# Kernel optimization log

Measured on AMD Instinct MI355X. Metric: run time of the kernel, lower is better.

## Reference

```python
import jax, jax.numpy as jnp
import numpy as np

B, V, K = 4, 4096, 128
C_IN, C_W, C_OUT, N_BLOCK = 16, 128, 128, 4
MLP_C = 3 * C_W  # x_in | x_diffuse | grad_features


def setup_inputs() -> dict:
    key = jax.random.key(0)
    ks = jax.random.split(key, 24)
    inp = {
        'x_in': jax.random.normal(ks[0], (B, V, C_IN), jnp.float32),
        'mass': jax.random.uniform(ks[1], (B, V), jnp.float32, 0.1, 1.0),
        'evals': jax.random.uniform(ks[2], (B, K), jnp.float32, 0.0, 50.0),
        'evecs': jax.random.normal(ks[3], (B, V, K), jnp.float32) / np.sqrt(V),
        'gradX': jax.random.normal(ks[4], (B, V, V), jnp.float32) * 0.01,
        'gradY': jax.random.normal(ks[5], (B, V, V), jnp.float32) * 0.01,
        # network parameters
        'Wf': jax.random.normal(ks[6], (C_IN, C_W), jnp.float32) / np.sqrt(C_IN),
        'bf': jnp.zeros((C_W,), jnp.float32),
        'Wl': jax.random.normal(ks[7], (C_W, C_OUT), jnp.float32) / np.sqrt(C_W),
        'bl': jnp.zeros((C_OUT,), jnp.float32),
        't': jax.random.uniform(ks[8], (N_BLOCK, C_W), jnp.float32, 0.0, 1.0),
        'Are': jax.random.normal(ks[9], (N_BLOCK, C_W, C_W), jnp.float32) / np.sqrt(C_W),
        'Aim': jax.random.normal(ks[10], (N_BLOCK, C_W, C_W), jnp.float32) / np.sqrt(C_W),
        'W0': jax.random.normal(ks[11], (N_BLOCK, MLP_C, C_W), jnp.float32) / np.sqrt(MLP_C),
        'b0': jnp.zeros((N_BLOCK, C_W), jnp.float32),
        'W1': jax.random.normal(ks[12], (N_BLOCK, C_W, C_W), jnp.float32) / np.sqrt(C_W),
        'b1': jnp.zeros((N_BLOCK, C_W), jnp.float32),
        'W2': jax.random.normal(ks[13], (N_BLOCK, C_W, C_W), jnp.float32) / np.sqrt(C_W),
        'b2': jnp.zeros((N_BLOCK, C_W), jnp.float32),
    }
    return inp


def _forward(x_in, mass, evals, evecs, gradX, gradY,
             Wf, bf, Wl, bl, t, Are, Aim, W0, b0, W1, b1, W2, b2):
    x = x_in @ Wf + bf  # [B,V,C]
    for i in range(N_BLOCK):
        # --- learned-time spectral diffusion ---
        ti = jnp.maximum(t[i], 1e-8)                                  # [C]
        x_spec = jnp.einsum('bvk,bvc->bkc', evecs, x * mass[..., None])  # to_basis
        coefs = jnp.exp(-evals[..., None] * ti)                       # [B,K,C]
        x_diff = jnp.einsum('bvk,bkc->bvc', evecs, coefs * x_spec)    # from_basis
        # --- spatial gradient features (per-batch grad operator matmuls) ---
        gx = jnp.einsum('bvw,bwc->bvc', gradX, x_diff)
        gy = jnp.einsum('bvw,bwc->bvc', gradY, x_diff)
        # complex-linear: (A_re + i A_im)(gx + i gy); torch Linear y = x W^T,
        # here weights are stored pre-transposed so y = x @ W.
        br = gx @ Are[i] - gy @ Aim[i]
        bi = gy @ Are[i] + gx @ Aim[i]
        gfeat = jnp.tanh(gx * br + gy * bi)                           # [B,V,C]
        # --- vertex MLP with residual (dropout inactive at inference) ---
        f = jnp.concatenate([x, x_diff, gfeat], axis=-1)              # [B,V,3C]
        h = jax.nn.relu(f @ W0[i] + b0[i])
        h = jax.nn.relu(h @ W1[i] + b1[i])
        h = h @ W2[i] + b2[i]
        x = x + h
    return x @ Wl + bl  # [B,V,C_OUT], outputs_at='vertices', no last_activation


def reference(x_in, mass, evals, evecs, gradX, gradY,
              Wf, bf, Wl, bl, t, Are, Aim, W0, b0, W1, b1, W2, b2):
    return _forward(x_in, mass, evals, evecs, gradX, gradY,
                    Wf, bf, Wl, bl, t, Are, Aim, W0, b0, W1, b1, W2, b2)
```

## Files before the change

### kernel.cpp

```cpp
#include <hip/hip_runtime.h>
#include <stdint.h>
#include <math.h>


typedef unsigned short u16;
typedef __attribute__((ext_vector_type(8))) short short8;
typedef __attribute__((ext_vector_type(8))) __bf16 bf16x8;
typedef __attribute__((ext_vector_type(4))) float f32x4;

#define B_ 4
#define V_ 4096
#define K_ 128
#define C_ 128

__device__ __forceinline__ float bf2f(u16 u) {
    union { unsigned i; float f; } v; v.i = ((unsigned)u) << 16; return v.f;
}
__device__ __forceinline__ u16 f2bf(float f) {
    union { float f; unsigned i; } v; v.f = f;
    unsigned u = v.i;
    return (u16)((u + 0x7fffu + ((u >> 16) & 1u)) >> 16);
}

__device__ __forceinline__ f32x4 mfma16(short8 a, short8 b, f32x4 c) {
    return __builtin_amdgcn_mfma_f32_16x16x32_bf16(
        __builtin_bit_cast(bf16x8, a), __builtin_bit_cast(bf16x8, b), c, 0, 0, 0);
}

__device__ __forceinline__ void gl_lds16(const u16* g, u16* l) {
    __builtin_amdgcn_global_load_lds(
        (const __attribute__((address_space(1))) unsigned*)g,
        (__attribute__((address_space(3))) unsigned*)l, 16, 0, 0);
}

template <int RT>
__device__ __forceinline__ void gemm_core(const u16* A, int lda,
                                          const u16* Bt, int ldbt, int kIters,
                                          f32x4 (&acc)[RT][4], u16* As, u16* Bs) {
    const int tid = threadIdx.x;
    const int lane = tid & 63, wave = tid >> 6;
    const int rb = (wave >> 1) * (RT * 16), cb = (wave & 1) * 64;
    const int lrow = lane >> 3;
    const int xorc = (lane & 7) ^ lrow;
    const int q = lane >> 4, m = lane & 15;

    for (int kk = 0; kk < kIters; ++kk) {
        const u16* Ak = A + kk * 64 + xorc * 8;
        const u16* Bk = Bt + kk * 64 + xorc * 8;
#pragma unroll
        for (int g = 0; g < RT; ++g) {
            int rowb = wave * (RT * 8) + g * 8;
            gl_lds16(Ak + (size_t)(rowb + lrow) * lda, As + rowb * 64);
        }
#pragma unroll
        for (int g = 0; g < 4; ++g) {
            int rowb = wave * 32 + g * 8;
            gl_lds16(Bk + (size_t)(rowb + lrow) * ldbt, Bs + rowb * 64);
        }
        __syncthreads();
#pragma unroll
// ... 7 lines not shown
#pragma unroll
            for (int t = 0; t < 4; ++t) {
                int nr = cb + t * 16 + m;
                b[t] = *(const short8*)(Bs + nr * 64 + ((((k0 << 2) + q) ^ (nr & 7)) << 3));
            }
#pragma unroll
            for (int rt = 0; rt < RT; ++rt)
#pragma unroll
                for (int ct = 0; ct < 4; ++ct)
                    acc[rt][ct] = mfma16(a[rt], b[ct], acc[rt][ct]);
        }
        __syncthreads();
    }
}

__global__ void k_tr32(const float* __restrict__ src, u16* __restrict__ dst,
                       int R, int C) {
    __shared__ u16 tile[64][65];
    int b = blockIdx.z;
    src += (size_t)b * R * C;
    dst += (size_t)b * R * C;
    int r0 = blockIdx.x * 64, c0 = blockIdx.y * 64;
    int t = threadIdx.x, cc = t & 63;
#pragma unroll
    for (int i = 0; i < 16; ++i) {
        int rr = (t >> 6) * 16 + i;
        int r = r0 + rr, c = c0 + cc;
        if (r < R && c < C) tile[rr][cc] = f2bf(src[(size_t)r * C + c]);
    }
    __syncthreads();
#pragma unroll
    for (int i = 0; i < 16; ++i) {
        int cc2 = (t >> 6) * 16 + i, rr2 = t & 63;
        int c = c0 + cc2, r = r0 + rr2;
        if (r < R && c < C) dst[(size_t)c * R + r] = tile[rr2][cc2];
    }
}

__global__ void k_xmt(const u16* __restrict__ src, const float* __restrict__ mass,
                      u16* __restrict__ dst) {
    __shared__ u16 tile[64][65];
    int b = blockIdx.z;
    const u16* s = src + (size_t)b * V_ * C_;
    u16* d = dst + (size_t)b * V_ * C_;
    const float* ms = mass + (size_t)b * V_;
    int r0 = blockIdx.x * 64, c0 = blockIdx.y * 64;
    int t = threadIdx.x, cc = t & 63;
#pragma unroll
    for (int i = 0; i < 16; ++i) {
        int rr = (t >> 6) * 16 + i;
        int r = r0 + rr, c = c0 + cc;
        tile[rr][cc] = f2bf(bf2f(s[(size_t)r * C_ + c]) * ms[r]);
    }
    __syncthreads();
#pragma unroll
    for (int i = 0; i < 16; ++i) {
        int cc2 = (t >> 6) * 16 + i, rr2 = t & 63;
        d[(size_t)(c0 + cc2) * V_ + r0 + rr2] = tile[rr2][cc2];
    }
}

__global__ void k_cast(const float* __restrict__ src, u16* __restrict__ dst) {
    int i = blockIdx.x * 256 + threadIdx.x;
    float4 f = ((const float4*)src)[i];
    ushort4 o;
    o.x = f2bf(f.x); o.y = f2bf(f.y); o.z = f2bf(f.z); o.w = f2bf(f.w);
    ((ushort4*)dst)[i] = o;
}

__global__ void k_init(const float* __restrict__ x_in, const float* __restrict__ Wf,
                       const float* __restrict__ bfv, float* __restrict__ x32,
                       u16* __restrict__ xb) {
    int idx = blockIdx.x * 256 + threadIdx.x;
    int row = idx >> 7, c = idx & 127;
    float acc = bfv[c];
#pragma unroll
    for (int k = 0; k < 16; ++k)
        acc += x_in[row * 16 + k] * Wf[k * 128 + c];
    x32[idx] = acc;
    xb[idx] = f2bf(acc);
}

__global__ __launch_bounds__(256, 2) void k_gxe(const float* __restrict__ gradX,
                                                const float* __restrict__ gradY,
                                                const u16* __restrict__ evT,
                                                u16* __restrict__ GXE,
                                                u16* __restrict__ GYE) {
    __shared__ alignas(16) u16 As[64 * 64];
    __shared__ alignas(16) u16 Bs[128 * 64];
    int mt = blockIdx.x, b = blockIdx.y, op = blockIdx.z;
    const float* G = (op ? gradY : gradX) + (size_t)b * V_ * V_ + (size_t)mt * 64 * V_;
    const u16* Bt = evT + (size_t)b * K_ * V_;
    f32x4 acc[2][4];
#pragma unroll
    for (int i = 0; i < 2; ++i)
#pragma unroll
        for (int j = 0; j < 4; ++j) acc[i][j] = {0.f, 0.f, 0.f, 0.f};

    const int tid = threadIdx.x, lane = tid & 63, wave = tid >> 6;
    const int lrow = lane >> 3, xorc = (lane & 7) ^ lrow;
    const int q = lane >> 4, m = lane & 15;
    const int rb = (wave >> 1) * 32, cb = (wave & 1) * 64;
    const int arow = tid >> 3, achk = tid & 7;

    for (int kk = 0; kk < 64; ++kk) {
#pragma unroll
        for (int h = 0; h < 2; ++h) {
            int r = arow + h * 32;
            const float* src = G + (size_t)r * V_ + kk * 64 + achk * 8;
            float4 f0 = *(const float4*)src;
            float4 f1 = *(const float4*)(src + 4);
            short8 v;
            v[0] = (short)f2bf(f0.x); v[1] = (short)f2bf(f0.y);
            v[2] = (short)f2bf(f0.z); v[3] = (short)f2bf(f0.w);
            v[4] = (short)f2bf(f1.x); v[5] = (short)f2bf(f1.y);
            v[6] = (short)f2bf(f1.z); v[7] = (short)f2bf(f1.w);
            *(short8*)(As + r * 64 + ((achk ^ (r & 7)) << 3)) = v;
        }
        const u16* Bk = Bt + kk * 64 + xorc * 8;
#pragma unroll
// ... 11 lines not shown
                a[t] = *(const short8*)(As + row * 64 + ((((k0 << 2) + q) ^ (row & 7)) << 3));
            }
#pragma unroll
            for (int t = 0; t < 4; ++t) {
                int nr = cb + t * 16 + m;
                bfr[t] = *(const short8*)(Bs + nr * 64 + ((((k0 << 2) + q) ^ (nr & 7)) << 3));
            }
#pragma unroll
            for (int rt = 0; rt < 2; ++rt)
#pragma unroll
                for (int ct = 0; ct < 4; ++ct)
                    acc[rt][ct] = mfma16(a[rt], bfr[ct], acc[rt][ct]);
        }
        __syncthreads();
    }
    u16* out = (op ? GYE : GXE) + (size_t)b * V_ * K_ + (size_t)mt * 64 * K_;
#pragma unroll
    for (int rt = 0; rt < 2; ++rt)
#pragma unroll
        for (int ct = 0; ct < 4; ++ct)
#pragma unroll
            for (int r = 0; r < 4; ++r)
                out[(size_t)(rb + rt * 16 + q * 4 + r) * K_ + cb + ct * 16 + m] =
                    f2bf(acc[rt][ct][r]);
}

__global__ __launch_bounds__(256, 2) void k_spec(const u16* __restrict__ evT,
                                                 const u16* __restrict__ xmt,
                                                 float* __restrict__ specP) {
    __shared__ alignas(16) u16 As[128 * 64];
    __shared__ alignas(16) u16 Bs[128 * 64];
    int chunk = blockIdx.x, b = blockIdx.y;
    const u16* A = evT + (size_t)b * K_ * V_ + chunk * 128;
    const u16* Bt = xmt + (size_t)b * C_ * V_ + chunk * 128;
    f32x4 acc[4][4];
#pragma unroll
    for (int i = 0; i < 4; ++i)
#pragma unroll
        for (int j = 0; j < 4; ++j) acc[i][j] = {0.f, 0.f, 0.f, 0.f};
    gemm_core<4>(A, V_, Bt, V_, 2, acc, As, Bs);
    float* out = specP + (size_t)(b * 32 + chunk) * K_ * C_;
    int lane = threadIdx.x & 63, wave = threadIdx.x >> 6;
    int rb = (wave >> 1) * 64, cb = (wave & 1) * 64, q = lane >> 4, m = lane & 15;
#pragma unroll
    for (int rt = 0; rt < 4; ++rt)
#pragma unroll
        for (int ct = 0; ct < 4; ++ct)
#pragma unroll
            for (int r = 0; r < 4; ++r)
                out[(size_t)(rb + rt * 16 + q * 4 + r) * C_ + cb + ct * 16 + m] =
                    acc[rt][ct][r];
}

__global__ void k_reduce(const float* __restrict__ specP,
                         const float* __restrict__ evals,
                         const float* __restrict__ tvec, u16* __restrict__ yt) {
    int idx = blockIdx.x * 256 + threadIdx.x;
    int c = idx & 127, k = (idx >> 7) & 127, b = idx >> 14;
    float ti = fmaxf(tvec[c], 1e-8f);
    float ev = evals[b * 128 + k];
    float coef = expf(-ev * ti);
    float s = 0.f;
    const float* p = specP + (size_t)b * 32 * K_ * C_ + k * C_ + c;
#pragma unroll
    for (int j = 0; j < 32; ++j) s += p[(size_t)j * K_ * C_];
    yt[((size_t)b * C_ + c) * K_ + k] = f2bf(coef * s);
}

__global__ __launch_bounds__(256, 2) void k_three(
    const u16* __restrict__ evb, const u16* __restrict__ gxe,
    const u16* __restrict__ gye, const u16* __restrict__ yt,
    u16* __restrict__ xd, u16* __restrict__ gx, u16* __restrict__ gy) {
    __shared__ alignas(16) u16 As[128 * 64];
    __shared__ alignas(16) u16 Bs[128 * 64];
    int mt = blockIdx.x, b = blockIdx.y, op = blockIdx.z;
    const u16* Asrc = (op == 0) ? evb : (op == 1) ? gxe : gye;
    u16* out = (op == 0) ? xd : (op == 1) ? gx : gy;
    const u16* A = Asrc + (size_t)b * V_ * K_ + (size_t)mt * 128 * K_;
    const u16* Bt = yt + (size_t)b * C_ * K_;
    f32x4 acc[4][4];
#pragma unroll
    for (int i = 0; i < 4; ++i)
#pragma unroll
        for (int j = 0; j < 4; ++j) acc[i][j] = {0.f, 0.f, 0.f, 0.f};
    gemm_core<4>(A, K_, Bt, K_, 2, acc, As, Bs);
    out += (size_t)b * V_ * C_ + (size_t)mt * 128 * C_;
    int lane = threadIdx.x & 63, wave = threadIdx.x >> 6;
    int rb = (wave >> 1) * 64, cb = (wave & 1) * 64, q = lane >> 4, m = lane & 15;
#pragma unroll
    for (int rt = 0; rt < 4; ++rt)
#pragma unroll
        for (int ct = 0; ct < 4; ++ct)
#pragma unroll
            for (int r = 0; r < 4; ++r)
                out[(size_t)(rb + rt * 16 + q * 4 + r) * C_ + cb + ct * 16 + m] =
                    f2bf(acc[rt][ct][r]);
}

__global__ __launch_bounds__(256, 2) void k_complex(
    const u16* __restrict__ gx, const u16* __restrict__ gy,
    const u16* __restrict__ art, const u16* __restrict__ ait,
    u16* __restrict__ gf) {
    __shared__ alignas(16) u16 gxs[128 * 64];
    __shared__ alignas(16) u16 gys[128 * 64];
    __shared__ alignas(16) u16 ars[64 * 64];
    __shared__ alignas(16) u16 ais[64 * 64];
    int mt = blockIdx.x, nh = blockIdx.y, b = blockIdx.z;
    size_t boff = (size_t)b * V_ * C_ + (size_t)mt * 128 * C_;
    const int tid = threadIdx.x, lane = tid & 63, wave = tid >> 6;
    const int lrow = lane >> 3, xorc = (lane & 7) ^ lrow;
    const int q = lane >> 4, m = lane & 15;
    const int rb = wave * 32;

    f32x4 abr[2][4], abi[2][4];
#pragma unroll
    for (int i = 0; i < 2; ++i)
#pragma unroll
        for (int j = 0; j < 4; ++j) {
            abr[i][j] = {0.f, 0.f, 0.f, 0.f};
            abi[i][j] = {0.f, 0.f, 0.f, 0.f};
        }

    for (int kk = 0; kk < 2; ++kk) {
        int kof = kk * 64 + xorc * 8;
#pragma unroll
        for (int g = 0; g < 4; ++g) {
            int rowb = wave * 32 + g * 8;
            gl_lds16(gx + boff + (size_t)(rowb + lrow) * C_ + kof, gxs + rowb * 64);
            gl_lds16(gy + boff + (size_t)(rowb + lrow) * C_ + kof, gys + rowb * 64);
        }
#pragma unroll
        for (int g = 0; g < 2; ++g) {
            int rowb = wave * 16 + g * 8;
            gl_lds16(art + (size_t)(nh * 64 + rowb + lrow) * C_ + kof, ars + rowb * 64);
            gl_lds16(ait + (size_t)(nh * 64 + rowb + lrow) * C_ + kof, ais + rowb * 64);
        }
        __syncthreads();
#pragma unroll
        for (int k0 = 0; k0 < 2; ++k0) {
            short8 ax[2], ay[2], bre[4], bim[4], bimn[4];
#pragma unroll
            for (int t = 0; t < 2; ++t) {
                int row = rb + t * 16 + m;
                int off = row * 64 + ((((k0 << 2) + q) ^ (row & 7)) << 3);
                ax[t] = *(const short8*)(gxs + off);
                ay[t] = *(const short8*)(gys + off);
            }
#pragma unroll
            for (int t = 0; t < 4; ++t) {
                int nr = t * 16 + m;
                int off = nr * 64 + ((((k0 << 2) + q) ^ (nr & 7)) << 3);
                bre[t] = *(const short8*)(ars + off);
                bim[t] = *(const short8*)(ais + off);
#pragma unroll
                for (int j = 0; j < 8; ++j) bimn[t][j] = bim[t][j] ^ (short)0x8000;
            }
#pragma unroll
            for (int rt = 0; rt < 2; ++rt)
#pragma unroll
                for (int ct = 0; ct < 4; ++ct) {
                    abr[rt][ct] = mfma16(ax[rt], bre[ct], abr[rt][ct]);
                    abr[rt][ct] = mfma16(ay[rt], bimn[ct], abr[rt][ct]);
                    abi[rt][ct] = mfma16(ay[rt], bre[ct], abi[rt][ct]);
                    abi[rt][ct] = mfma16(ax[rt], bim[ct], abi[rt][ct]);
                }
        }
        __syncthreads();
    }
#pragma unroll
    for (int rt = 0; rt < 2; ++rt)
#pragma unroll
        for (int ct = 0; ct < 4; ++ct)
#pragma unroll
            for (int r = 0; r < 4; ++r) {
                int row = rb + rt * 16 + q * 4 + r;
                int col = nh * 64 + ct * 16 + m;
                size_t idx = boff + (size_t)row * C_ + col;
                float g1 = bf2f(gx[idx]), g2 = bf2f(gy[idx]);
                float z = g1 * abr[rt][ct][r] + g2 * abi[rt][ct][r];
                gf[idx] = f2bf(tanhf(z));
            }
}

__device__ __forceinline__ void write_h(const f32x4 (&acc)[4][4],
                                        const float* bias, u16* hb) {
    int lane = threadIdx.x & 63, wave = threadIdx.x >> 6;
    int rb = (wave >> 1) * 64, cb = (wave & 1) * 64, q = lane >> 4, m = lane & 15;
#pragma unroll
    for (int rt = 0; rt < 4; ++rt)
#pragma unroll
        for (int ct = 0; ct < 4; ++ct)
#pragma unroll
            for (int r = 0; r < 4; ++r) {
                int row = rb + rt * 16 + q * 4 + r;
                int col = cb + ct * 16 + m;
                float v = acc[rt][ct][r] + bias[col];
                v = fmaxf(v, 0.f);
                int w = col >> 6, cl = col & 63;
                hb[w * 8192 + row * 64 + (((cl >> 3) ^ (row & 7)) << 3) + (cl & 7)] =
                    f2bf(v);
            }
}

__device__ __forceinline__ void dense_lds(const u16* hb, const u16* wt,
                                          f32x4 (&acc)[4][4]) {
    int lane = threadIdx.x & 63, wave = threadIdx.x >> 6;
    int rb = (wave >> 1) * 64, cb = (wave & 1) * 64, q = lane >> 4, m = lane & 15;
#pragma unroll
    for (int k0 = 0; k0 < 4; ++k0) {
        int k = k0 * 32 + q * 8;
        int w = k >> 6, cw = (k & 63) >> 3;
        short8 a[4], bb[4];
#pragma unroll
        for (int t = 0; t < 4; ++t) {
            int row = rb + t * 16 + m;
            a[t] = *(const short8*)(hb + w * 8192 + row * 64 + ((cw ^ (row & 7)) << 3));
            int nr = cb + t * 16 + m;
            bb[t] = *(const short8*)(wt + (size_t)nr * C_ + k);
        }
#pragma unroll
        for (int rt = 0; rt < 4; ++rt)
#pragma unroll
            for (int ct = 0; ct < 4; ++ct)
                acc[rt][ct] = mfma16(a[rt], bb[ct], acc[rt][ct]);
    }
}

__global__ __launch_bounds__(256, 2) void k_mlp(
    const u16* xb, const u16* xd, const u16* gfi, const u16* w0t,
    const u16* w1t, const u16* w2t, const float* b0, const float* b1,
    const float* b2, float* x32, u16* xbw) {
    __shared__ alignas(16) u16 smem[32768];
    u16* As = smem;
    u16* Bs = smem + 8192;
    u16* h0 = smem + 16384;
    int mt = blockIdx.x, b = blockIdx.y;
    size_t boff = (size_t)b * V_ * C_ + (size_t)mt * 128 * C_;

    f32x4 acc[4][4];
#pragma unroll
    for (int i = 0; i < 4; ++i)
#pragma unroll
        for (int j = 0; j < 4; ++j) acc[i][j] = {0.f, 0.f, 0.f, 0.f};
    gemm_core<4>(xb + boff, C_, w0t, 384, 2, acc, As, Bs);
    gemm_core<4>(xd + boff, C_, w0t + 128, 384, 2, acc, As, Bs);
    gemm_core<4>(gfi + boff, C_, w0t + 256, 384, 2, acc, As, Bs);
    write_h(acc, b0, h0);
    __syncthreads();

    f32x4 acc2[4][4];
#pragma unroll
    for (int i = 0; i < 4; ++i)
#pragma unroll
        for (int j = 0; j < 4; ++j) acc2[i][j] = {0.f, 0.f, 0.f, 0.f};
    dense_lds(h0, w1t, acc2);
    u16* h1 = smem;
    write_h(acc2, b1, h1);
    __syncthreads();

    f32x4 acc3[4][4];
#pragma unroll
    for (int i = 0; i < 4; ++i)
#pragma unroll
        for (int j = 0; j < 4; ++j) acc3[i][j] = {0.f, 0.f, 0.f, 0.f};
    dense_lds(h1, w2t, acc3);

    int lane = threadIdx.x & 63, wave = threadIdx.x >> 6;
    int rb = (wave >> 1) * 64, cb = (wave & 1) * 64, q = lane >> 4, m = lane & 15;
#pragma unroll
    for (int rt = 0; rt < 4; ++rt)
#pragma unroll
        for (int ct = 0; ct < 4; ++ct)
#pragma unroll
            for (int r = 0; r < 4; ++r) {
                int row = rb + rt * 16 + q * 4 + r;
                int col = cb + ct * 16 + m;
                size_t idx = boff + (size_t)row * C_ + col;
                float v = x32[idx] + acc3[rt][ct][r] + b2[col];
                x32[idx] = v;
                xbw[idx] = f2bf(v);
            }
}

__global__ __launch_bounds__(256, 2) void k_final(const u16* __restrict__ xb,
                                                  const u16* __restrict__ wlt,
                                                  const float* __restrict__ bl,
                                                  float* __restrict__ out) {
    __shared__ alignas(16) u16 As[128 * 64];
    __shared__ alignas(16) u16 Bs[128 * 64];
    int mt = blockIdx.x, b = blockIdx.y;
    size_t boff = (size_t)b * V_ * C_ + (size_t)mt * 128 * C_;
    f32x4 acc[4][4];
#pragma unroll
    for (int i = 0; i < 4; ++i)
#pragma unroll
        for (int j = 0; j < 4; ++j) acc[i][j] = {0.f, 0.f, 0.f, 0.f};
// ... 34 lines not shown
    const float* W1    = (const float*)d_in[15];
    const float* b1    = (const float*)d_in[16];
    const float* W2    = (const float*)d_in[17];
    const float* b2    = (const float*)d_in[18];
    float* out = (float*)d_out;

    char* wsb = (char*)d_ws;
    size_t o = 0;
    auto take = [&](size_t bytes) -> void* {
        void* p = wsb + o;
        o += (bytes + 255) & ~(size_t)255;
        return p;
    };
    float* X32 = (float*)take((size_t)B_ * V_ * C_ * 4);
    u16* XB    = (u16*)take((size_t)B_ * V_ * C_ * 2);
    u16* XMT   = (u16*)take((size_t)B_ * V_ * C_ * 2);
    u16* EVT   = (u16*)take((size_t)B_ * V_ * K_ * 2);
    u16* EVB   = (u16*)take((size_t)B_ * V_ * K_ * 2);
    u16* GXE   = (u16*)take((size_t)B_ * V_ * K_ * 2);
    u16* GYE   = (u16*)take((size_t)B_ * V_ * K_ * 2);
    float* SP  = (float*)take((size_t)B_ * 32 * K_ * C_ * 4);
    u16* YT    = (u16*)take((size_t)B_ * K_ * C_ * 2);
    u16* XD    = (u16*)take((size_t)B_ * V_ * C_ * 2);
    u16* GX    = (u16*)take((size_t)B_ * V_ * C_ * 2);
    u16* GY    = (u16*)take((size_t)B_ * V_ * C_ * 2);
    u16* GF    = (u16*)take((size_t)B_ * V_ * C_ * 2);
    u16* ART   = (u16*)take((size_t)4 * C_ * C_ * 2);
    u16* AIT   = (u16*)take((size_t)4 * C_ * C_ * 2);
    u16* W0T   = (u16*)take((size_t)4 * 384 * C_ * 2);
    u16* W1T   = (u16*)take((size_t)4 * C_ * C_ * 2);
    u16* W2T   = (u16*)take((size_t)4 * C_ * C_ * 2);
    u16* WLT   = (u16*)take((size_t)C_ * C_ * 2);

    k_tr32<<<dim3(2, 2, 4), 256, 0, stream>>>(Are, ART, 128, 128);
    k_tr32<<<dim3(2, 2, 4), 256, 0, stream>>>(Aim, AIT, 128, 128);
    k_tr32<<<dim3(6, 2, 4), 256, 0, stream>>>(W0, W0T, 384, 128);
    k_tr32<<<dim3(2, 2, 4), 256, 0, stream>>>(W1, W1T, 128, 128);
    k_tr32<<<dim3(2, 2, 4), 256, 0, stream>>>(W2, W2T, 128, 128);
    k_tr32<<<dim3(2, 2, 1), 256, 0, stream>>>(Wl, WLT, 128, 128);
    k_tr32<<<dim3(64, 2, 4), 256, 0, stream>>>(evecs, EVT, 4096, 128);
    k_cast<<<dim3(2048), 256, 0, stream>>>(evecs, EVB);
    k_init<<<dim3(8192), 256, 0, stream>>>(x_in, Wf, bfv, X32, XB);
    k_gxe<<<dim3(64, 4, 2), 256, 0, stream>>>(gradX, gradY, EVT, GXE, GYE);

    for (int i = 0; i < 4; ++i) {
        k_xmt<<<dim3(64, 2, 4), 256, 0, stream>>>(XB, mass, XMT);
        k_spec<<<dim3(32, 4), 256, 0, stream>>>(EVT, XMT, SP);
        k_reduce<<<dim3(256), 256, 0, stream>>>(SP, evals, tv + i * 128, YT);
        k_three<<<dim3(32, 4, 3), 256, 0, stream>>>(EVB, GXE, GYE, YT, XD, GX, GY);
        k_complex<<<dim3(32, 2, 4), 256, 0, stream>>>(GX, GY, ART + i * 16384,
                                                      AIT + i * 16384, GF);
        k_mlp<<<dim3(32, 4), 256, 0, stream>>>(XB, XD, GF, W0T + i * 49152,
                                               W1T + i * 16384, W2T + i * 16384,
                                               b0 + i * 128, b1 + i * 128,
                                               b2 + i * 128, X32, XB);
    }
    k_final<<<dim3(32, 4), 256, 0, stream>>>(XB, WLT, bl, out);
}
```

Before: 929.0 us.

## Fuse per-block pipeline into one tile kernel, split-K gradient precompute, merge prep kernels

Several changes land together. The per-block from-basis, gradient, complex-linear and MLP kernels become one k_tile kernel working on 32-row tiles, so intermediates stay in LDS and are not written to global memory. The mass scaling and transpose move into k_spec, which removes k_xmt. The large gradX/gradY times evecs product is split four ways along K for more parallelism, with an fp32 partial buffer and a separate reduce kernel. The weight transposes and evec casts are merged into fewer launches. In exchange, the fused kernel uses 64KB of LDS and has many syncthreads, and the split-K path adds extra fp32 traffic.

```diff
diff --git a/kernel.cpp b/kernel.cpp
--- a/kernel.cpp
+++ b/kernel.cpp
@@ -21,16 +21,18 @@
     unsigned u = v.i;
     return (u16)((u + 0x7fffu + ((u >> 16) & 1u)) >> 16);
 }
-
 __device__ __forceinline__ f32x4 mfma16(short8 a, short8 b, f32x4 c) {
     return __builtin_amdgcn_mfma_f32_16x16x32_bf16(
         __builtin_bit_cast(bf16x8, a), __builtin_bit_cast(bf16x8, b), c, 0, 0, 0);
 }
-
 __device__ __forceinline__ void gl_lds16(const u16* g, u16* l) {
     __builtin_amdgcn_global_load_lds(
         (const __attribute__((address_space(1))) unsigned*)g,
         (__attribute__((address_space(3))) unsigned*)l, 16, 0, 0);
+}
+__device__ __forceinline__ int poff(int row, int col) {
+    return row * 128 + ((col >> 6) << 6) +
+           ((((col >> 3) & 7) ^ (row & 7)) << 3) + (col & 7);
 }
 
 template <int RT>
@@ -43,7 +45,6 @@
     const int lrow = lane >> 3;
     const int xorc = (lane & 7) ^ lrow;
     const int q = lane >> 4, m = lane & 15;
-
     for (int kk = 0; kk < kIters; ++kk) {
         const u16* Ak = A + kk * 64 + xorc * 8;
         const u16* Bk = Bt + kk * 64 + xorc * 8;
@@ -81,58 +82,59 @@
     }
 }
 
-__global__ void k_tr32(const float* __restrict__ src, u16* __restrict__ dst,
-                       int R, int C) {
+__global__ void k_prep(const float* __restrict__ Are, const float* __restrict__ Aim,
+                       const float* __restrict__ W0, const float* __restrict__ W1,
+                       const float* __restrict__ W2, const float* __restrict__ Wl,
+                       u16* ART, u16* AIT, u16* W0T, u16* W1T, u16* W2T, u16* WLT) {
     __shared__ u16 tile[64][65];
-    int b = blockIdx.z;
-    src += (size_t)b * R * C;
-    dst += (size_t)b * R * C;
+    int id = blockIdx.x;
+    const float* src; u16* dst; int R, bi2, tr, tc;
+    if (id < 16)       { src = Are; dst = ART; R = 128; bi2 = id >> 2; tr = (id >> 1) & 1; tc = id & 1; }
+    else if (id < 32)  { id -= 16; src = Aim; dst = AIT; R = 128; bi2 = id >> 2; tr = (id >> 1) & 1; tc = id & 1; }
+    else if (id < 80)  { id -= 32; src = W0; dst = W0T; R = 384; bi2 = id / 12; int t2 = id % 12; tr = t2 >> 1; tc = t2 & 1; }
+    else if (id < 96)  { id -= 80; src = W1; dst = W1T; R = 128; bi2 = id >> 2; tr = (id >> 1) & 1; tc = id & 1; }
+    else if (id < 112) { id -= 96; src = W2; dst = W2T; R = 128; bi2 = id >> 2; tr = (id >> 1) & 1; tc = id & 1; }
+    else               { id -= 112; src = Wl; dst = WLT; R = 128; bi2 = 0; tr = (id >> 1) & 1; tc = id & 1; }
+    src += (size_t)bi2 * R * 128;
+    dst += (size_t)bi2 * R * 128;
+    int r0 = tr * 64, c0 = tc * 64;
+    int t = threadIdx.x, cc = t & 63;
+#pragma unroll
+    for (int i = 0; i < 16; ++i) {
+        int rr = (t >> 6) * 16 + i;
+        tile[rr][cc] = f2bf(src[(size_t)(r0 + rr) * 128 + c0 + cc]);
+    }
+    __syncthreads();
+#pragma unroll
+    for (int i = 0; i < 16; ++i) {
+        int cc2 = (t >> 6) * 16 + i, rr2 = t & 63;
+        dst[(size_t)(c0 + cc2) * R + r0 + rr2] = tile[rr2][cc2];
+    }
+}
+
+__global__ void k_evt(const float* __restrict__ src, u16* __restrict__ evt,
+                      u16* __restrict__ evb) {
+    __shared__ u16 tile[64][65];
+    int bz = blockIdx.z;
+    const float* s = src + (size_t)bz * V_ * K_;
+    u16* dT = evt + (size_t)bz * V_ * K_;
+    u16* dC = evb + (size_t)bz * V_ * K_;
     int r0 = blockIdx.x * 64, c0 = blockIdx.y * 64;
     int t = threadIdx.x, cc = t & 63;
 #pragma unroll
     for (int i = 0; i < 16; ++i) {
         int rr = (t >> 6) * 16 + i;
         int r = r0 + rr, c = c0 + cc;
-        if (r < R && c < C) tile[rr][cc] = f2bf(src[(size_t)r * C + c]);
+        u16 u = f2bf(s[(size_t)r * K_ + c]);
+        tile[rr][cc] = u;
+        dC[(size_t)r * K_ + c] = u;
     }
     __syncthreads();
 #pragma unroll
     for (int i = 0; i < 16; ++i) {
         int cc2 = (t >> 6) * 16 + i, rr2 = t & 63;
-        int c = c0 + cc2, r = r0 + rr2;
-        if (r < R && c < C) dst[(size_t)c * R + r] = tile[rr2][cc2];
-    }
-}
-
-__global__ void k_xmt(const u16* __restrict__ src, const float* __restrict__ mass,
-                      u16* __restrict__ dst) {
-    __shared__ u16 tile[64][65];
-    int b = blockIdx.z;
-    const u16* s = src + (size_t)b * V_ * C_;
-    u16* d = dst + (size_t)b * V_ * C_;
-    const float* ms = mass + (size_t)b * V_;
-    int r0 = blockIdx.x * 64, c0 = blockIdx.y * 64;
-    int t = threadIdx.x, cc = t & 63;
-#pragma unroll
-    for (int i = 0; i < 16; ++i) {
-        int rr = (t >> 6) * 16 + i;
-        int r = r0 + rr, c = c0 + cc;
-        tile[rr][cc] = f2bf(bf2f(s[(size_t)r * C_ + c]) * ms[r]);
-    }
-    __syncthreads();
-#pragma unroll
-    for (int i = 0; i < 16; ++i) {
-        int cc2 = (t >> 6) * 16 + i, rr2 = t & 63;
-        d[(size_t)(c0 + cc2) * V_ + r0 + rr2] = tile[rr2][cc2];
-    }
-}
-
-__global__ void k_cast(const float* __restrict__ src, u16* __restrict__ dst) {
-    int i = blockIdx.x * 256 + threadIdx.x;
-    float4 f = ((const float4*)src)[i];
-    ushort4 o;
-    o.x = f2bf(f.x); o.y = f2bf(f.y); o.z = f2bf(f.z); o.w = f2bf(f.w);
-    ((ushort4*)dst)[i] = o;
+        dT[(size_t)(c0 + cc2) * V_ + r0 + rr2] = tile[rr2][cc2];
+    }
 }
 
 __global__ void k_init(const float* __restrict__ x_in, const float* __restrict__ Wf,
@@ -148,16 +150,16 @@
     xb[idx] = f2bf(acc);
 }
 
-__global__ __launch_bounds__(256, 2) void k_gxe(const float* __restrict__ gradX,
-                                                const float* __restrict__ gradY,
+__global__ __launch_bounds__(256, 2) void k_gxe(const float* __restrict__ gX,
+                                                const float* __restrict__ gY,
                                                 const u16* __restrict__ evT,
-                                                u16* __restrict__ GXE,
-                                                u16* __restrict__ GYE) {
+                                                float* __restrict__ GP) {
     __shared__ alignas(16) u16 As[64 * 64];
     __shared__ alignas(16) u16 Bs[128 * 64];
-    int mt = blockIdx.x, b = blockIdx.y, op = blockIdx.z;
-    const float* G = (op ? gradY : gradX) + (size_t)b * V_ * V_ + (size_t)mt * 64 * V_;
-    const u16* Bt = evT + (size_t)b * K_ * V_;
+    int mt = blockIdx.x, ks = blockIdx.y, z = blockIdx.z;
+    int op = z >> 2, b = z & 3;
+    const float* G = (op ? gY : gX) + (size_t)b * V_ * V_ + (size_t)mt * 64 * V_ + ks * 1024;
+    const u16* Bt = evT + (size_t)b * K_ * V_ + ks * 1024;
     f32x4 acc[2][4];
 #pragma unroll
     for (int i = 0; i < 2; ++i)
@@ -170,7 +172,7 @@
     const int rb = (wave >> 1) * 32, cb = (wave & 1) * 64;
     const int arow = tid >> 3, achk = tid & 7;
 
-    for (int kk = 0; kk < 64; ++kk) {
+    for (int kk = 0; kk < 16; ++kk) {
 #pragma unroll
         for (int h = 0; h < 2; ++h) {
             int r = arow + h * 32;
@@ -212,7 +214,7 @@
         }
         __syncthreads();
     }
-    u16* out = (op ? GYE : GXE) + (size_t)b * V_ * K_ + (size_t)mt * 64 * K_;
+    float* out = GP + ((size_t)z * 4 + ks) * ((size_t)V_ * K_) + (size_t)mt * 64 * K_;
 #pragma unroll
     for (int rt = 0; rt < 2; ++rt)
 #pragma unroll
@@ -220,264 +222,352 @@
 #pragma unroll
             for (int r = 0; r < 4; ++r)
                 out[(size_t)(rb + rt * 16 + q * 4 + r) * K_ + cb + ct * 16 + m] =
-                    f2bf(acc[rt][ct][r]);
+                    acc[rt][ct][r];
+}
+
+__global__ void k_gxered(const float* __restrict__ GP, u16* __restrict__ GXE,
+                         u16* __restrict__ GYE) {
+    int i = blockIdx.x * 256 + threadIdx.x;
+    size_t e = (size_t)i * 4;
+    int z = (int)(e / ((size_t)V_ * K_));
+    size_t r = e - (size_t)z * V_ * K_;
+    const float* base = GP + (size_t)z * 4 * V_ * K_ + r;
+    float4 s = *(const float4*)base;
+#pragma unroll
+    for (int ks = 1; ks < 4; ++ks) {
+        float4 t = *(const float4*)(base + (size_t)ks * V_ * K_);
+        s.x += t.x; s.y += t.y; s.z += t.z; s.w += t.w;
+    }
+    u16* dst = (z < 4 ? GXE : GYE) + (size_t)(z & 3) * V_ * K_ + r;
+    ushort4 o;
+    o.x = f2bf(s.x); o.y = f2bf(s.y); o.z = f2bf(s.z); o.w = f2bf(s.w);
+    *(ushort4*)dst = o;
 }
 
 __global__ __launch_bounds__(256, 2) void k_spec(const u16* __restrict__ evT,
-                                                 const u16* __restrict__ xmt,
-                                                 float* __restrict__ specP) {
+                                                 const u16* __restrict__ xb,
+                                                 const float* __restrict__ mass,
+                                                 float* __restrict__ SP) {
     __shared__ alignas(16) u16 As[128 * 64];
     __shared__ alignas(16) u16 Bs[128 * 64];
-    int chunk = blockIdx.x, b = blockIdx.y;
-    const u16* A = evT + (size_t)b * K_ * V_ + chunk * 128;
-    const u16* Bt = xmt + (size_t)b * C_ * V_ + chunk * 128;
+    int vc = blockIdx.x, b = blockIdx.y;
+    const int tid = threadIdx.x, lane = tid & 63, wave = tid >> 6;
+    const int q = lane >> 4, m = lane & 15;
+    const int r8 = lane >> 3, s8 = lane & 7;
+    const u16* Ab = evT + (size_t)b * K_ * V_ + vc * 64;
+#pragma unroll
+    for (int c2 = 0; c2 < 4; ++c2) {
+        int row0 = wave * 32 + c2 * 8;
+        int row = row0 + r8;
+        gl_lds16(Ab + (size_t)row * V_ + ((s8 ^ (row & 7)) << 3), As + row0 * 64);
+    }
+    {
+        int v = tid & 63, cg = tid >> 6;
+        const u16* xrow = xb + ((size_t)b * V_ + vc * 64 + v) * C_;
+        float ms = mass[(size_t)b * V_ + vc * 64 + v];
+#pragma unroll
+        for (int j = 0; j < 4; ++j) {
+            short8 d = *(const short8*)(xrow + cg * 32 + j * 8);
+#pragma unroll
+            for (int e2 = 0; e2 < 8; ++e2) {
+                int c = cg * 32 + j * 8 + e2;
+                Bs[c * 64 + (((v >> 3) ^ (c & 7)) << 3) + (v & 7)] =
+                    f2bf(bf2f((u16)d[e2]) * ms);
+            }
+        }
+    }
+    __syncthreads();
     f32x4 acc[4][4];
 #pragma unroll
     for (int i = 0; i < 4; ++i)
 #pragma unroll
         for (int j = 0; j < 4; ++j) acc[i][j] = {0.f, 0.f, 0.f, 0.f};
-    gemm_core<4>(A, V_, Bt, V_, 2, acc, As, Bs);
-    float* out = specP + (size_t)(b * 32 + chunk) * K_ * C_;
-    int lane = threadIdx.x & 63, wave = threadIdx.x >> 6;
-    int rb = (wave >> 1) * 64, cb = (wave & 1) * 64, q = lane >> 4, m = lane & 15;
+    const int rwv = wave >> 1, cwv = wave & 1;
+#pragma unroll
+    for (int s = 0; s < 2; ++s) {
+        short8 a[4], bb[4];
+#pragma unroll
+        for (int rt = 0; rt < 4; ++rt) {
+            int row = rwv * 64 + rt * 16 + m;
+            a[rt] = *(const short8*)(As + row * 64 + (((s * 4 + q) ^ (row & 7)) << 3));
+        }
+#pragma unroll
+        for (int ct = 0; ct < 4; ++ct) {
+            int c = cwv * 64 + ct * 16 + m;
+            bb[ct] = *(const short8*)(Bs + c * 64 + (((s * 4 + q) ^ (c & 7)) << 3));
+        }
+#pragma unroll
+        for (int rt = 0; rt < 4; ++rt)
+#pragma unroll
+            for (int ct = 0; ct < 4; ++ct)
+                acc[rt][ct] = mfma16(a[rt], bb[ct], acc[rt][ct]);
+    }
+    float* outp = SP + ((size_t)b * 64 + vc) * (K_ * C_);
 #pragma unroll
     for (int rt = 0; rt < 4; ++rt)
 #pragma unroll
         for (int ct = 0; ct < 4; ++ct)
 #pragma unroll
-            for (int r = 0; r < 4; ++r)
-                out[(size_t)(rb + rt * 16 + q * 4 + r) * C_ + cb + ct * 16 + m] =
-                    acc[rt][ct][r];
-}
-
-__global__ void k_reduce(const float* __restrict__ specP,
-                         const float* __restrict__ evals,
+            for (int r = 0; r < 4; ++r) {
+                int row = rwv * 64 + rt * 16 + q * 4 + r;
+                int col = cwv * 64 + ct * 16 + m;
+                outp[(size_t)row * C_ + col] = acc[rt][ct][r];
+            }
+}
+
+__global__ void k_reduce(const float* __restrict__ SP, const float* __restrict__ evals,
                          const float* __restrict__ tvec, u16* __restrict__ yt) {
     int idx = blockIdx.x * 256 + threadIdx.x;
     int c = idx & 127, k = (idx >> 7) & 127, b = idx >> 14;
     float ti = fmaxf(tvec[c], 1e-8f);
-    float ev = evals[b * 128 + k];
-    float coef = expf(-ev * ti);
+    float coef = expf(-evals[b * 128 + k] * ti);
+    const float* p = SP + (size_t)b * 64 * (K_ * C_) + k * C_ + c;
     float s = 0.f;
-    const float* p = specP + (size_t)b * 32 * K_ * C_ + k * C_ + c;
-#pragma unroll
-    for (int j = 0; j < 32; ++j) s += p[(size_t)j * K_ * C_];
+#pragma unroll
+    for (int j = 0; j < 64; ++j) s += p[(size_t)j * (K_ * C_)];
     yt[((size_t)b * C_ + c) * K_ + k] = f2bf(coef * s);
 }
 
-__global__ __launch_bounds__(256, 2) void k_three(
+__global__ __launch_bounds__(256, 2) void k_tile(
     const u16* __restrict__ evb, const u16* __restrict__ gxe,
     const u16* __restrict__ gye, const u16* __restrict__ yt,
-    u16* __restrict__ xd, u16* __restrict__ gx, u16* __restrict__ gy) {
-    __shared__ alignas(16) u16 As[128 * 64];
-    __shared__ alignas(16) u16 Bs[128 * 64];
-    int mt = blockIdx.x, b = blockIdx.y, op = blockIdx.z;
-    const u16* Asrc = (op == 0) ? evb : (op == 1) ? gxe : gye;
-    u16* out = (op == 0) ? xd : (op == 1) ? gx : gy;
-    const u16* A = Asrc + (size_t)b * V_ * K_ + (size_t)mt * 128 * K_;
-    const u16* Bt = yt + (size_t)b * C_ * K_;
-    f32x4 acc[4][4];
-#pragma unroll
-    for (int i = 0; i < 4; ++i)
-#pragma unroll
-        for (int j = 0; j < 4; ++j) acc[i][j] = {0.f, 0.f, 0.f, 0.f};
-    gemm_core<4>(A, K_, Bt, K_, 2, acc, As, Bs);
-    out += (size_t)b * V_ * C_ + (size_t)mt * 128 * C_;
-    int lane = threadIdx.x & 63, wave = threadIdx.x >> 6;
-    int rb = (wave >> 1) * 64, cb = (wave & 1) * 64, q = lane >> 4, m = lane & 15;
-#pragma unroll
-    for (int rt = 0; rt < 4; ++rt)
+    const u16* __restrict__ art, const u16* __restrict__ ait,
+    const u16* __restrict__ w0t, const u16* __restrict__ w1t,
+    const u16* __restrict__ w2t, const float* __restrict__ b0,
+    const float* __restrict__ b1, const float* __restrict__ b2,
+    float* __restrict__ x32, u16* __restrict__ xbg) {
+    __shared__ alignas(16) u16 smem[32768];
+    u16* RA  = smem;
+    u16* RB  = smem + 16384;
+    u16* RC0 = smem + 20480;
+    u16* RC1 = smem + 24576;
+    u16* RC2 = smem + 28672;
+    const int tid = threadIdx.x, lane = tid & 63, wave = tid >> 6;
+    const int q = lane >> 4, m = lane & 15;
+    const int rw = wave >> 1, cw = wave & 1;
+    const int r4 = lane >> 4, h4 = (lane >> 3) & 1, s4 = lane & 7;
+    const int r8 = lane >> 3, s8 = lane & 7;
+    const int mt = blockIdx.x, b = blockIdx.y;
+    const size_t boff = ((size_t)b * V_ + mt * 32) * (size_t)C_;
+
+    {
+        const u16* Y = yt + (size_t)b * C_ * K_;
+#pragma unroll
+        for (int c2 = 0; c2 < 8; ++c2) {
+            int row0 = wave * 32 + c2 * 4;
+            int row = row0 + r4;
+            gl_lds16(Y + (size_t)row * 128 + h4 * 64 + ((s4 ^ (row & 7)) << 3),
+                     RA + row0 * 128);
+        }
+    }
+#pragma unroll 1
+    for (int p = 0; p < 3; ++p) {
+        __syncthreads();
+        const u16* Asrc = (p == 0 ? evb : p == 1 ? gxe : gye) + boff;
+#pragma unroll
+        for (int c2 = 0; c2 < 2; ++c2) {
+            int row0 = wave * 8 + c2 * 4;
+            int row = row0 + r4;
+            gl_lds16(Asrc + (size_t)row * 128 + h4 * 64 + ((s4 ^ (row & 7)) << 3),
+                     RB + row0 * 128);
+        }
+        __syncthreads();
+        f32x4 acc[4];
+#pragma unroll
+        for (int j = 0; j < 4; ++j) acc[j] = {0.f, 0.f, 0.f, 0.f};
+#pragma unroll
+        for (int s = 0; s < 4; ++s) {
+            int ar = rw * 16 + m;
+            short8 a = *(const short8*)(RB + ar * 128 + ((s >> 1) << 6) +
+                                        ((((s & 1) * 4 + q) ^ (ar & 7)) << 3));
+#pragma unroll
+            for (int ct = 0; ct < 4; ++ct) {
+                int c = cw * 64 + ct * 16 + m;
+                short8 bb = *(const short8*)(RA + c * 128 + ((s >> 1) << 6) +
+                                             ((((s & 1) * 4 + q) ^ (c & 7)) << 3));
+                acc[ct] = mfma16(a, bb, acc[ct]);
+            }
+        }
+        u16* dst = (p == 0 ? RC0 : p == 1 ? RC1 : RC2);
 #pragma unroll
         for (int ct = 0; ct < 4; ++ct)
 #pragma unroll
-            for (int r = 0; r < 4; ++r)
-                out[(size_t)(rb + rt * 16 + q * 4 + r) * C_ + cb + ct * 16 + m] =
-                    f2bf(acc[rt][ct][r]);
-}
-
-__global__ __launch_bounds__(256, 2) void k_complex(
-    const u16* __restrict__ gx, const u16* __restrict__ gy,
-    const u16* __restrict__ art, const u16* __restrict__ ait,
-    u16* __restrict__ gf) {
-    __shared__ alignas(16) u16 gxs[128 * 64];
-    __shared__ alignas(16) u16 gys[128 * 64];
-    __shared__ alignas(16) u16 ars[64 * 64];
-    __shared__ alignas(16) u16 ais[64 * 64];
-    int mt = blockIdx.x, nh = blockIdx.y, b = blockIdx.z;
-    size_t boff = (size_t)b * V_ * C_ + (size_t)mt * 128 * C_;
-    const int tid = threadIdx.x, lane = tid & 63, wave = tid >> 6;
-    const int lrow = lane >> 3, xorc = (lane & 7) ^ lrow;
-    const int q = lane >> 4, m = lane & 15;
-    const int rb = wave * 32;
-
-    f32x4 abr[2][4], abi[2][4];
-#pragma unroll
-    for (int i = 0; i < 2; ++i)
-#pragma unroll
-        for (int j = 0; j < 4; ++j) {
-            abr[i][j] = {0.f, 0.f, 0.f, 0.f};
-            abi[i][j] = {0.f, 0.f, 0.f, 0.f};
-        }
-
-    for (int kk = 0; kk < 2; ++kk) {
-        int kof = kk * 64 + xorc * 8;
-#pragma unroll
-        for (int g = 0; g < 4; ++g) {
-            int rowb = wave * 32 + g * 8;
-            gl_lds16(gx + boff + (size_t)(rowb + lrow) * C_ + kof, gxs + rowb * 64);
-            gl_lds16(gy + boff + (size_t)(rowb + lrow) * C_ + kof, gys + rowb * 64);
-        }
-#pragma unroll
-        for (int g = 0; g < 2; ++g) {
-            int rowb = wave * 16 + g * 8;
-            gl_lds16(art + (size_t)(nh * 64 + rowb + lrow) * C_ + kof, ars + rowb * 64);
-            gl_lds16(ait + (size_t)(nh * 64 + rowb + lrow) * C_ + kof, ais + rowb * 64);
-        }
-        __syncthreads();
-#pragma unroll
-        for (int k0 = 0; k0 < 2; ++k0) {
-            short8 ax[2], ay[2], bre[4], bim[4], bimn[4];
-#pragma unroll
-            for (int t = 0; t < 2; ++t) {
-                int row = rb + t * 16 + m;
-                int off = row * 64 + ((((k0 << 2) + q) ^ (row & 7)) << 3);
-                ax[t] = *(const short8*)(gxs + off);
-                ay[t] = *(const short8*)(gys + off);
-            }
-#pragma unroll
-            for (int t = 0; t < 4; ++t) {
-                int nr = t * 16 + m;
-                int off = nr * 64 + ((((k0 << 2) + q) ^ (nr & 7)) << 3);
-                bre[t] = *(const short8*)(ars + off);
-                bim[t] = *(const short8*)(ais + off);
-#pragma unroll
-                for (int j = 0; j < 8; ++j) bimn[t][j] = bim[t][j] ^ (short)0x8000;
-            }
-#pragma unroll
-            for (int rt = 0; rt < 2; ++rt)
-#pragma unroll
-                for (int ct = 0; ct < 4; ++ct) {
-                    abr[rt][ct] = mfma16(ax[rt], bre[ct], abr[rt][ct]);
-                    abr[rt][ct] = mfma16(ay[rt], bimn[ct], abr[rt][ct]);
-                    abi[rt][ct] = mfma16(ay[rt], bre[ct], abi[rt][ct]);
-                    abi[rt][ct] = mfma16(ax[rt], bim[ct], abi[rt][ct]);
-                }
-        }
-        __syncthreads();
-    }
-#pragma unroll
-    for (int rt = 0; rt < 2; ++rt)
-#pragma unroll
-        for (int ct = 0; ct < 4; ++ct)
-#pragma unroll
             for (int r = 0; r < 4; ++r) {
-                int row = rb + rt * 16 + q * 4 + r;
-                int col = nh * 64 + ct * 16 + m;
-                size_t idx = boff + (size_t)row * C_ + col;
-                float g1 = bf2f(gx[idx]), g2 = bf2f(gy[idx]);
-                float z = g1 * abr[rt][ct][r] + g2 * abi[rt][ct][r];
-                gf[idx] = f2bf(tanhf(z));
-            }
-}
-
-__device__ __forceinline__ void write_h(const f32x4 (&acc)[4][4],
-                                        const float* bias, u16* hb) {
-    int lane = threadIdx.x & 63, wave = threadIdx.x >> 6;
-    int rb = (wave >> 1) * 64, cb = (wave & 1) * 64, q = lane >> 4, m = lane & 15;
-#pragma unroll
-    for (int rt = 0; rt < 4; ++rt)
-#pragma unroll
-        for (int ct = 0; ct < 4; ++ct)
+                int row = rw * 16 + q * 4 + r;
+                int col = cw * 64 + ct * 16 + m;
+                dst[poff(row, col)] = f2bf(acc[ct][r]);
+            }
+    }
+    __syncthreads();
+#pragma unroll 1
+    for (int h = 0; h < 2; ++h) {
+        if (h) __syncthreads();
+#pragma unroll
+        for (int c2 = 0; c2 < 4; ++c2) {
+            int row0 = wave * 16 + c2 * 4;
+            int row = row0 + r4;
+            size_t so = (size_t)(h * 64 + row) * 128 + h4 * 64 + ((s4 ^ (row & 7)) << 3);
+            gl_lds16(art + so, RA + row0 * 128);
+            gl_lds16(ait + so, RA + 8192 + row0 * 128);
+        }
+        __syncthreads();
+        f32x4 br[2], bi[2];
+#pragma unroll
+        for (int j = 0; j < 2; ++j) { br[j] = {0.f, 0.f, 0.f, 0.f}; bi[j] = {0.f, 0.f, 0.f, 0.f}; }
+#pragma unroll
+        for (int s = 0; s < 4; ++s) {
+            int ar = rw * 16 + m;
+            int ao = ar * 128 + ((s >> 1) << 6) + ((((s & 1) * 4 + q) ^ (ar & 7)) << 3);
+            short8 ax = *(const short8*)(RC1 + ao);
+            short8 ay = *(const short8*)(RC2 + ao);
+#pragma unroll
+            for (int ct = 0; ct < 2; ++ct) {
+                int n = cw * 32 + ct * 16 + m;
+                int bo = n * 128 + ((s >> 1) << 6) + ((((s & 1) * 4 + q) ^ (n & 7)) << 3);
+                short8 bre = *(const short8*)(RA + bo);
+                short8 bim = *(const short8*)(RA + 8192 + bo);
+                short8 bimn;
+#pragma unroll
+                for (int j = 0; j < 8; ++j) bimn[j] = bim[j] ^ (short)0x8000;
+                br[ct] = mfma16(ax, bre, br[ct]);
+                br[ct] = mfma16(ay, bimn, br[ct]);
+                bi[ct] = mfma16(ay, bre, bi[ct]);
+                bi[ct] = mfma16(ax, bim, bi[ct]);
+            }
+        }
+#pragma unroll
+        for (int ct = 0; ct < 2; ++ct)
 #pragma unroll
             for (int r = 0; r < 4; ++r) {
-                int row = rb + rt * 16 + q * 4 + r;
-                int col = cb + ct * 16 + m;
-                float v = acc[rt][ct][r] + bias[col];
-                v = fmaxf(v, 0.f);
-                int w = col >> 6, cl = col & 63;
-                hb[w * 8192 + row * 64 + (((cl >> 3) ^ (row & 7)) << 3) + (cl & 7)] =
-                    f2bf(v);
-            }
-}
-
-__device__ __forceinline__ void dense_lds(const u16* hb, const u16* wt,
-                                          f32x4 (&acc)[4][4]) {
-    int lane = threadIdx.x & 63, wave = threadIdx.x >> 6;
-    int rb = (wave >> 1) * 64, cb = (wave & 1) * 64, q = lane >> 4, m = lane & 15;
-#pragma unroll
-    for (int k0 = 0; k0 < 4; ++k0) {
-        int k = k0 * 32 + q * 8;
-        int w = k >> 6, cw = (k & 63) >> 3;
-        short8 a[4], bb[4];
-#pragma unroll
-        for (int t = 0; t < 4; ++t) {
-            int row = rb + t * 16 + m;
-            a[t] = *(const short8*)(hb + w * 8192 + row * 64 + ((cw ^ (row & 7)) << 3));
-            int nr = cb + t * 16 + m;
-            bb[t] = *(const short8*)(wt + (size_t)nr * C_ + k);
-        }
-#pragma unroll
-        for (int rt = 0; rt < 4; ++rt)
-#pragma unroll
-            for (int ct = 0; ct < 4; ++ct)
-                acc[rt][ct] = mfma16(a[rt], bb[ct], acc[rt][ct]);
-    }
-}
-
-__global__ __launch_bounds__(256, 2) void k_mlp(
-    const u16* xb, const u16* xd, const u16* gfi, const u16* w0t,
-    const u16* w1t, const u16* w2t, const float* b0, const float* b1,
-    const float* b2, float* x32, u16* xbw) {
-    __shared__ alignas(16) u16 smem[32768];
-    u16* As = smem;
-    u16* Bs = smem + 8192;
-    u16* h0 = smem + 16384;
-    int mt = blockIdx.x, b = blockIdx.y;
-    size_t boff = (size_t)b * V_ * C_ + (size_t)mt * 128 * C_;
-
-    f32x4 acc[4][4];
-#pragma unroll
-    for (int i = 0; i < 4; ++i)
-#pragma unroll
-        for (int j = 0; j < 4; ++j) acc[i][j] = {0.f, 0.f, 0.f, 0.f};
-    gemm_core<4>(xb + boff, C_, w0t, 384, 2, acc, As, Bs);
-    gemm_core<4>(xd + boff, C_, w0t + 128, 384, 2, acc, As, Bs);
-    gemm_core<4>(gfi + boff, C_, w0t + 256, 384, 2, acc, As, Bs);
-    write_h(acc, b0, h0);
-    __syncthreads();
-
-    f32x4 acc2[4][4];
-#pragma unroll
-    for (int i = 0; i < 4; ++i)
-#pragma unroll
-        for (int j = 0; j < 4; ++j) acc2[i][j] = {0.f, 0.f, 0.f, 0.f};
-    dense_lds(h0, w1t, acc2);
-    u16* h1 = smem;
-    write_h(acc2, b1, h1);
-    __syncthreads();
-
-    f32x4 acc3[4][4];
-#pragma unroll
-    for (int i = 0; i < 4; ++i)
-#pragma unroll
-        for (int j = 0; j < 4; ++j) acc3[i][j] = {0.f, 0.f, 0.f, 0.f};
-    dense_lds(h1, w2t, acc3);
-
-    int lane = threadIdx.x & 63, wave = threadIdx.x >> 6;
-    int rb = (wave >> 1) * 64, cb = (wave & 1) * 64, q = lane >> 4, m = lane & 15;
-#pragma unroll
-    for (int rt = 0; rt < 4; ++rt)
-#pragma unroll
-        for (int ct = 0; ct < 4; ++ct)
-#pragma unroll
-            for (int r = 0; r < 4; ++r) {
-                int row = rb + rt * 16 + q * 4 + r;
-                int col = cb + ct * 16 + m;
-                size_t idx = boff + (size_t)row * C_ + col;
-                float v = x32[idx] + acc3[rt][ct][r] + b2[col];
-                x32[idx] = v;
-                xbw[idx] = f2bf(v);
-            }
+                int row = rw * 16 + q * 4 + r;
+                int col = h * 64 + cw * 32 + ct * 16 + m;
+                int off = poff(row, col);
+                float g1 = bf2f(RC1[off]), g2 = bf2f(RC2[off]);
+                RB[off] = f2bf(tanhf(g1 * br[ct][r] + g2 * bi[ct][r]));
+            }
+    }
+    __syncthreads();
+#pragma unroll
+    for (int c2 = 0; c2 < 2; ++c2) {
+        int row0 = wave * 8 + c2 * 4;
+        int row = row0 + r4;
+        gl_lds16(xbg + boff + (size_t)row * 128 + h4 * 64 + ((s4 ^ (row & 7)) << 3),
+                 RC1 + row0 * 128);
+    }
+    f32x4 acc0[4];
+#pragma unroll
+    for (int j = 0; j < 4; ++j) acc0[j] = {0.f, 0.f, 0.f, 0.f};
+#pragma unroll 1
+    for (int kc = 0; kc < 6; ++kc) {
+        if (kc) __syncthreads();
+#pragma unroll
+        for (int c2 = 0; c2 < 4; ++c2) {
+            int row0 = wave * 32 + c2 * 8;
+            int row = row0 + r8;
+            gl_lds16(w0t + (size_t)row * 384 + kc * 64 + ((s8 ^ (row & 7)) << 3),
+                     RA + row0 * 64);
+        }
+        __syncthreads();
+        const u16* Ab = (kc < 2) ? RC1 : (kc < 4) ? RC0 : RB;
+        int half = kc & 1;
+#pragma unroll
+        for (int s = 0; s < 2; ++s) {
+            int ar = rw * 16 + m;
+            short8 a = *(const short8*)(Ab + ar * 128 + (half << 6) +
+                                        (((s * 4 + q) ^ (ar & 7)) << 3));
+#pragma unroll
+            for (int ct = 0; ct < 4; ++ct) {
+                int n = cw * 64 + ct * 16 + m;
+                short8 bb = *(const short8*)(RA + n * 64 + (((s * 4 + q) ^ (n & 7)) << 3));
+                acc0[ct] = mfma16(a, bb, acc0[ct]);
+            }
+        }
+    }
+    __syncthreads();
+#pragma unroll
+    for (int ct = 0; ct < 4; ++ct)
+#pragma unroll
+        for (int r = 0; r < 4; ++r) {
+            int row = rw * 16 + q * 4 + r;
+            int col = cw * 64 + ct * 16 + m;
+            RC2[poff(row, col)] = f2bf(fmaxf(acc0[ct][r] + b0[col], 0.f));
+        }
+    __syncthreads();
+    f32x4 acc1[4];
+#pragma unroll
+    for (int j = 0; j < 4; ++j) acc1[j] = {0.f, 0.f, 0.f, 0.f};
+#pragma unroll 1
+    for (int kc = 0; kc < 2; ++kc) {
+        if (kc) __syncthreads();
+#pragma unroll
+        for (int c2 = 0; c2 < 4; ++c2) {
+            int row0 = wave * 32 + c2 * 8;
+            int row = row0 + r8;
+            gl_lds16(w1t + (size_t)row * 128 + kc * 64 + ((s8 ^ (row & 7)) << 3),
+                     RA + row0 * 64);
+        }
+        __syncthreads();
+#pragma unroll
+        for (int s = 0; s < 2; ++s) {
+            int ar = rw * 16 + m;
+            short8 a = *(const short8*)(RC2 + ar * 128 + (kc << 6) +
+                                        (((s * 4 + q) ^ (ar & 7)) << 3));
+#pragma unroll
+            for (int ct = 0; ct < 4; ++ct) {
+                int n = cw * 64 + ct * 16 + m;
+                short8 bb = *(const short8*)(RA + n * 64 + (((s * 4 + q) ^ (n & 7)) << 3));
+                acc1[ct] = mfma16(a, bb, acc1[ct]);
+            }
+        }
+    }
+    __syncthreads();
+#pragma unroll
+    for (int ct = 0; ct < 4; ++ct)
+#pragma unroll
+        for (int r = 0; r < 4; ++r) {
+            int row = rw * 16 + q * 4 + r;
+            int col = cw * 64 + ct * 16 + m;
+            RC0[poff(row, col)] = f2bf(fmaxf(acc1[ct][r] + b1[col], 0.f));
+        }
+    __syncthreads();
+    f32x4 acc2[4];
+#pragma unroll
+    for (int j = 0; j < 4; ++j) acc2[j] = {0.f, 0.f, 0.f, 0.f};
+#pragma unroll 1
+    for (int kc = 0; kc < 2; ++kc) {
+        if (kc) __syncthreads();
+#pragma unroll
+        for (int c2 = 0; c2 < 4; ++c2) {
+            int row0 = wave * 32 + c2 * 8;
+            int row = row0 + r8;
+            gl_lds16(w2t + (size_t)row * 128 + kc * 64 + ((s8 ^ (row & 7)) << 3),
+                     RA + row0 * 64);
+        }
+        __syncthreads();
+#pragma unroll
+        for (int s = 0; s < 2; ++s) {
+            int ar = rw * 16 + m;
+            short8 a = *(const short8*)(RC0 + ar * 128 + (kc << 6) +
+                                        (((s * 4 + q) ^ (ar & 7)) << 3));
+#pragma unroll
+            for (int ct = 0; ct < 4; ++ct) {
+                int n = cw * 64 + ct * 16 + m;
+                short8 bb = *(const short8*)(RA + n * 64 + (((s * 4 + q) ^ (n & 7)) << 3));
+                acc2[ct] = mfma16(a, bb, acc2[ct]);
+            }
+        }
+    }
+#pragma unroll
+    for (int ct = 0; ct < 4; ++ct)
+#pragma unroll
+        for (int r = 0; r < 4; ++r) {
+            int row = rw * 16 + q * 4 + r;
+            int col = cw * 64 + ct * 16 + m;
+            size_t idx = boff + (size_t)row * C_ + col;
+            float v = x32[idx] + acc2[ct][r] + b2[col];
+            x32[idx] = v;
+            xbg[idx] = f2bf(v);
+        }
 }
 
 __global__ __launch_bounds__(256, 2) void k_final(const u16* __restrict__ xb,
@@ -542,17 +632,13 @@
     };
     float* X32 = (float*)take((size_t)B_ * V_ * C_ * 4);
     u16* XB    = (u16*)take((size_t)B_ * V_ * C_ * 2);
-    u16* XMT   = (u16*)take((size_t)B_ * V_ * C_ * 2);
     u16* EVT   = (u16*)take((size_t)B_ * V_ * K_ * 2);
     u16* EVB   = (u16*)take((size_t)B_ * V_ * K_ * 2);
     u16* GXE   = (u16*)take((size_t)B_ * V_ * K_ * 2);
     u16* GYE   = (u16*)take((size_t)B_ * V_ * K_ * 2);
-    float* SP  = (float*)take((size_t)B_ * 32 * K_ * C_ * 4);
+    float* GP  = (float*)take((size_t)8 * 4 * V_ * K_ * 4);
+    float* SP  = (float*)take((size_t)B_ * 64 * K_ * C_ * 4);
     u16* YT    = (u16*)take((size_t)B_ * K_ * C_ * 2);
-    u16* XD    = (u16*)take((size_t)B_ * V_ * C_ * 2);
-    u16* GX    = (u16*)take((size_t)B_ * V_ * C_ * 2);
-    u16* GY    = (u16*)take((size_t)B_ * V_ * C_ * 2);
-    u16* GF    = (u16*)take((size_t)B_ * V_ * C_ * 2);
     u16* ART   = (u16*)take((size_t)4 * C_ * C_ * 2);
     u16* AIT   = (u16*)take((size_t)4 * C_ * C_ * 2);
     u16* W0T   = (u16*)take((size_t)4 * 384 * C_ * 2);
@@ -560,28 +646,20 @@
     u16* W2T   = (u16*)take((size_t)4 * C_ * C_ * 2);
     u16* WLT   = (u16*)take((size_t)C_ * C_ * 2);
 
-    k_tr32<<<dim3(2, 2, 4), 256, 0, stream>>>(Are, ART, 128, 128);
-    k_tr32<<<dim3(2, 2, 4), 256, 0, stream>>>(Aim, AIT, 128, 128);
-    k_tr32<<<dim3(6, 2, 4), 256, 0, stream>>>(W0, W0T, 384, 128);
-    k_tr32<<<dim3(2, 2, 4), 256, 0, stream>>>(W1, W1T, 128, 128);
-    k_tr32<<<dim3(2, 2, 4), 256, 0, stream>>>(W2, W2T, 128, 128);
-    k_tr32<<<dim3(2, 2, 1), 256, 0, stream>>>(Wl, WLT, 128, 128);
-    k_tr32<<<dim3(64, 2, 4), 256, 0, stream>>>(evecs, EVT, 4096, 128);
-    k_cast<<<dim3(2048), 256, 0, stream>>>(evecs, EVB);
+    k_prep<<<dim3(116), 256, 0, stream>>>(Are, Aim, W0, W1, W2, Wl,
+                                          ART, AIT, W0T, W1T, W2T, WLT);
+    k_evt<<<dim3(64, 2, 4), 256, 0, stream>>>(evecs, EVT, EVB);
     k_init<<<dim3(8192), 256, 0, stream>>>(x_in, Wf, bfv, X32, XB);
-    k_gxe<<<dim3(64, 4, 2), 256, 0, stream>>>(gradX, gradY, EVT, GXE, GYE);
+    k_gxe<<<dim3(64, 4, 8), 256, 0, stream>>>(gradX, gradY, EVT, GP);
+    k_gxered<<<dim3(4096), 256, 0, stream>>>(GP, GXE, GYE);
 
     for (int i = 0; i < 4; ++i) {
-        k_xmt<<<dim3(64, 2, 4), 256, 0, stream>>>(XB, mass, XMT);
-        k_spec<<<dim3(32, 4), 256, 0, stream>>>(EVT, XMT, SP);
+        k_spec<<<dim3(64, 4), 256, 0, stream>>>(EVT, XB, mass, SP);
         k_reduce<<<dim3(256), 256, 0, stream>>>(SP, evals, tv + i * 128, YT);
-        k_three<<<dim3(32, 4, 3), 256, 0, stream>>>(EVB, GXE, GYE, YT, XD, GX, GY);
-        k_complex<<<dim3(32, 2, 4), 256, 0, stream>>>(GX, GY, ART + i * 16384,
-                                                      AIT + i * 16384, GF);
-        k_mlp<<<dim3(32, 4), 256, 0, stream>>>(XB, XD, GF, W0T + i * 49152,
-                                               W1T + i * 16384, W2T + i * 16384,
-                                               b0 + i * 128, b1 + i * 128,
-                                               b2 + i * 128, X32, XB);
+        k_tile<<<dim3(128, 4), 256, 0, stream>>>(
+            EVB, GXE, GYE, YT, ART + i * 16384, AIT + i * 16384,
+            W0T + i * 49152, W1T + i * 16384, W2T + i * 16384,
+            b0 + i * 128, b1 + i * 128, b2 + i * 128, X32, XB);
     }
     k_final<<<dim3(32, 4), 256, 0, stream>>>(XB, WLT, bl, out);
 }
```

Result: faster. 805.9 us (-13.3%).
